# Kernel tuning notes

Hardware: AMD Instinct MI355X
Metric: run time of the kernel (lower is better)

The kernel has to match this reference:

```python
import jax, jax.numpy as jnp
import numpy as np

B, L, DIM, H = 2, 2048, 1024, 16
HD = DIM // H  # head dim = 64
MASK_SCALE = -10 * 6  # faithful to the original source: mask_expand *= -10 * 6


def setup_inputs() -> dict:
    key = jax.random.key(0)
    ks = jax.random.split(key, 8)
    s = 1.0 / np.sqrt(DIM)
    return {
        "x": jax.random.normal(ks[0], (B, L, DIM), jnp.float32),
        "attention_mask": jax.random.uniform(ks[1], (B, L, L), jnp.float32),
        "Wq": jax.random.normal(ks[2], (DIM, DIM), jnp.float32) * s,
        "bq": jnp.zeros((DIM,), jnp.float32),
        "Wk": jax.random.normal(ks[3], (DIM, DIM), jnp.float32) * s,
        "bk": jnp.zeros((DIM,), jnp.float32),
        "Wv": jax.random.normal(ks[4], (DIM, DIM), jnp.float32) * s,
        "bv": jnp.zeros((DIM,), jnp.float32),
    }


def _split_heads(t):
    # [B, L, DIM] -> [B, H, L, HD]
    return t.reshape(B, L, H, HD).transpose(0, 2, 1, 3)


def reference(x, attention_mask, Wq, bq, Wk, bk, Wv, bv):
    q = _split_heads(x @ Wq + bq)
    k = _split_heads(x @ Wk + bk)
    v = _split_heads(x @ Wv + bv)
    scale = float(HD) ** -0.5
    # full [B, H, L, L] score matrix, as in the original
    scores = jnp.einsum("bhqd,bhkd->bhqk", q, k) * scale
    scores = scores + attention_mask[:, None, :, :] * MASK_SCALE
    probs = jax.nn.softmax(scores, axis=-1)
    ctx = jnp.einsum("bhqk,bhkd->bhqd", probs, v)
    # merge heads back: [B, L, DIM]
    return ctx.transpose(0, 2, 1, 3).reshape(B, L, DIM)
```

## Files before the change

kernel.cpp:

```cpp
#include <hip/hip_runtime.h>

#define LL 2048
#define NHEADS 16
#define HDIM 64
#define QSCALE 0.18033688011112042f
#define MASKC1 -86.56170245333780f

typedef __attribute__((ext_vector_type(8))) __bf16 bf16x8;
typedef __attribute__((ext_vector_type(4))) float f32x4;

__device__ __forceinline__ unsigned short f2bf(float f) {
  unsigned int u = __builtin_bit_cast(unsigned int, f);
  u += 0x7fffu + ((u >> 16) & 1u);
  return (unsigned short)(u >> 16);
}

__device__ __forceinline__ bf16x8 ld_frag(const unsigned short* p) {
  return *reinterpret_cast<const bf16x8*>(p);
}

__device__ __forceinline__ void async_cp16(const unsigned short* g, unsigned short* l) {
  __builtin_amdgcn_global_load_lds(
      (const __attribute__((address_space(1))) unsigned int*)(unsigned long long)(g),
      (__attribute__((address_space(3))) unsigned int*)(unsigned int)(unsigned long long)(l),
      16, 0, 0);
}

__global__ __launch_bounds__(256) void prep_kernel(
    const float* __restrict__ x, const float* __restrict__ Wq, const float* __restrict__ Wk,
    const float* __restrict__ Wv, unsigned short* __restrict__ xb,
    unsigned short* __restrict__ WtAll) {
  __shared__ float t[64][65];
  int blk = blockIdx.x;
  if (blk < 4096) {
    int i = (blk * 256 + threadIdx.x) * 4;
    float4 v = *reinterpret_cast<const float4*>(x + i);
    ushort4 o;
    o.x = f2bf(v.x); o.y = f2bf(v.y); o.z = f2bf(v.z); o.w = f2bf(v.w);
    *reinterpret_cast<ushort4*>(xb + i) = o;
  } else {
    int idx = blk - 4096;
    int z = idx >> 8; idx &= 255;
    const float* W = (z == 0) ? Wq : (z == 1) ? Wk : Wv;
    unsigned short* dst = WtAll + (size_t)z * 1024 * 1024;
    int n0 = (idx & 15) * 64, k0 = (idx >> 4) * 64;
    int tx = threadIdx.x & 63, ty = threadIdx.x >> 6;
#pragma unroll
    for (int p = 0; p < 16; ++p) {
      int kr = p * 4 + ty;
      t[kr][tx] = W[(size_t)(k0 + kr) * 1024 + n0 + tx];
    }
    __syncthreads();
#pragma unroll
    for (int p = 0; p < 16; ++p) {
      int nr = p * 4 + ty;
      dst[(size_t)(n0 + nr) * 1024 + k0 + tx] = f2bf(t[tx][nr]);
    }
  }
}

__global__ __launch_bounds__(256) void em_prep_kernel(const float* __restrict__ mask,
                                                      unsigned short* __restrict__ em) {
  int row = blockIdx.y;
  int t = blockIdx.x * 256 + threadIdx.x;
  int kb = t >> 4, c = t & 15;
  const float* src = mask + (size_t)row * LL + kb * 64 + c;
  ushort4 o;
  o.x = f2bf(__builtin_amdgcn_exp2f(src[0]  * MASKC1));
  o.y = f2bf(__builtin_amdgcn_exp2f(src[16] * MASKC1));
  o.z = f2bf(__builtin_amdgcn_exp2f(src[32] * MASKC1));
  o.w = f2bf(__builtin_amdgcn_exp2f(src[48] * MASKC1));
  *reinterpret_cast<ushort4*>(em + (size_t)row * LL + kb * 64 + 4 * c) = o;
}

__global__ __launch_bounds__(256) void qkv_gemm_kernel(
    const unsigned short* __restrict__ xb, const unsigned short* __restrict__ WtAll,
    const float* __restrict__ bq, const float* __restrict__ bk, const float* __restrict__ bv,
    unsigned short* __restrict__ qkv) {
  const int z = blockIdx.z;
  const unsigned short* Wt = WtAll + (size_t)z * 1024 * 1024;
  const float* bias = (z == 0) ? bq : (z == 1) ? bk : bv;
  unsigned short* outb = qkv + (size_t)z * 4194304;

  __shared__ __align__(16) unsigned short smem[16384];
  unsigned short* As = smem;
  unsigned short* Bs = smem + 8192;

  const int tid = threadIdx.x;
  const int w = tid >> 6, lane = tid & 63, g = lane >> 4, cc = lane & 15;
  const int wm = w >> 1, wn = w & 1;
  const int m0 = blockIdx.y * 128, n0 = blockIdx.x * 128;
  const int srow = lane >> 3;
  const int gc = ((lane & 7) - srow) & 7;
  const unsigned short* ga = xb + (size_t)(m0 + w * 32 + srow) * 1024 + gc * 8;
  const unsigned short* gb = Wt + (size_t)(n0 + w * 32 + srow) * 1024 + gc * 8;
  unsigned short* la = As + w * 2048;
  unsigned short* lb = Bs + w * 2048;

  f32x4 acc[4][4];
#pragma unroll
  for (int i = 0; i < 4; ++i)
#pragma unroll
    for (int j = 0; j < 4; ++j) acc[i][j] = (f32x4)0.0f;

  for (int kk = 0; kk < 1024; kk += 64) {
    __syncthreads();
#pragma unroll
    for (int i = 0; i < 4; ++i) {
      async_cp16(ga + i * 8192 + kk, la + i * 512);
      async_cp16(gb + i * 8192 + kk, lb + i * 512);
    }
    __syncthreads();
    bf16x8 af[4][2], bfr[4][2];
#pragma unroll
    for (int mt = 0; mt < 4; ++mt)
#pragma unroll
      for (int ks = 0; ks < 2; ++ks)
        af[mt][ks] = ld_frag(&As[(wm * 64 + mt * 16 + cc) * 64 + ((4 * ks + g + cc) & 7) * 8]);
#pragma unroll
    for (int nt = 0; nt < 4; ++nt)
#pragma unroll
      for (int ks = 0; ks < 2; ++ks)
        bfr[nt][ks] = ld_frag(&Bs[(wn * 64 + nt * 16 + cc) * 64 + ((4 * ks + g + cc) & 7) * 8]);
#pragma unroll
    for (int mt = 0; mt < 4; ++mt)
#pragma unroll
      for (int nt = 0; nt < 4; ++nt)
#pragma unroll
        for (int ks = 0; ks < 2; ++ks)
          acc[mt][nt] = __builtin_amdgcn_mfma_f32_16x16x32_bf16(af[mt][ks], bfr[nt][ks],
                                                                acc[mt][nt], 0, 0, 0);
  }

  if (z != 2) {
    const float sc = (z == 0) ? QSCALE : 1.0f;
#pragma unroll
    for (int nt = 0; nt < 4; ++nt) {
      int n = n0 + wn * 64 + nt * 16 + cc;
      float bval = bias[n];
      int h = n >> 6, d = n & 63;
#pragma unroll
      for (int mt = 0; mt < 4; ++mt) {
#pragma unroll
        for (int r = 0; r < 4; ++r) {
          int m = m0 + wm * 64 + mt * 16 + g * 4 + r;
          int b = m >> 11, l = m & 2047;
          outb[(((size_t)(b * NHEADS + h) * LL) + l) * HDIM + d] =
              f2bf((acc[mt][nt][r] + bval) * sc);
        }
      }
    }
  } else {
    __syncthreads();
#pragma unroll
    for (int nt = 0; nt < 4; ++nt) {
      int nr = wn * 64 + nt * 16 + cc;
      float bval = bias[n0 + nr];
#pragma unroll
      for (int mt = 0; mt < 4; ++mt)
#pragma unroll
        for (int r = 0; r < 4; ++r)
          smem[nr * 128 + wm * 64 + 16 * g + 4 * r + mt] = f2bf(acc[mt][nt][r] + bval);
    }
    __syncthreads();
    int row = tid >> 1, half = tid & 1;
    int n = n0 + row, hh = n >> 6, dd = n & 63;
    int bb = m0 >> 11, l0 = (m0 & 2047) + half * 64;
    unsigned short* dst = outb + ((size_t)(bb * NHEADS + hh) * HDIM + dd) * LL + l0;
#pragma unroll
    for (int i = 0; i < 8; ++i)
      *reinterpret_cast<uint4*>(dst + i * 8) =
          *reinterpret_cast<const uint4*>(&smem[row * 128 + half * 64 + i * 8]);
  }
}

__global__ __launch_bounds__(256, 4) void flash_kernel(
    const unsigned short* __restrict__ Qb, const unsigned short* __restrict__ Kb,
    const unsigned short* __restrict__ Vt, const unsigned short* __restrict__ Em,
    float* __restrict__ out) {
  const int bh = blockIdx.y, b = bh >> 4, h = bh & 15;
  const int q0 = blockIdx.x * 64;
  const int tid = threadIdx.x, w = tid >> 6, lane = tid & 63, g = lane >> 4, cc = lane & 15;
  const size_t bhoff = (size_t)bh * LL * HDIM;

  __shared__ __align__(16) unsigned short Ps[64 * 64];
  __shared__ __align__(16) unsigned short Ks[2][64 * 64];
  __shared__ __align__(16) unsigned short Vs[2][64 * 64];

  bf16x8 aq[2];
#pragma unroll
  for (int ks = 0; ks < 2; ++ks)
    aq[ks] = *reinterpret_cast<const bf16x8*>(
        Qb + bhoff + (size_t)(q0 + w * 16 + cc) * HDIM + ks * 32 + g * 8);

  const int srow = lane >> 3;
  const int gcs = ((lane & 7) - srow) & 7;
  const unsigned short* kg0 = Kb + bhoff + (size_t)(w * 8 + srow) * HDIM + gcs * 8;
  const unsigned short* kg1 = Kb + bhoff + (size_t)(32 + w * 8 + srow) * HDIM + gcs * 8;
  const unsigned short* vg0 = Vt + bhoff + (size_t)(w * 8 + srow) * LL + gcs * 8;
  const unsigned short* vg1 = Vt + bhoff + (size_t)(32 + w * 8 + srow) * LL + gcs * 8;

  float li[4];
  f32x4 oacc[4];
#pragma unroll
  for (int r = 0; r < 4; ++r) li[r] = 0.0f;
#pragma unroll
  for (int nt = 0; nt < 4; ++nt) oacc[nt] = (f32x4)0.0f;

  const unsigned short* embase = Em + ((size_t)b * LL + q0 + w * 16) * LL + 4 * cc;

  async_cp16(kg0, Ks[0] + w * 512);
  async_cp16(kg1, Ks[0] + (w + 4) * 512);
  async_cp16(vg0, Vs[0] + w * 512);
  async_cp16(vg1, Vs[0] + (w + 4) * 512);

#pragma unroll 2
  for (int kt = 0; kt < 32; ++kt) {
    const int buf = kt & 1;
    __syncthreads();
    if (kt + 1 < 32) {
      const int nb = buf ^ 1;
      async_cp16(kg0 + (size_t)(kt + 1) * 64 * HDIM, Ks[nb] + w * 512);
      async_cp16(kg1 + (size_t)(kt + 1) * 64 * HDIM, Ks[nb] + (w + 4) * 512);
      async_cp16(vg0 + (kt + 1) * 64, Vs[nb] + w * 512);
      async_cp16(vg1 + (kt + 1) * 64, Vs[nb] + (w + 4) * 512);
    }
    uint2 emv[4];
#pragma unroll
    for (int r = 0; r < 4; ++r)
      emv[r] = *reinterpret_cast<const uint2*>(embase + (size_t)(g * 4 + r) * LL + kt * 64);

    bf16x8 bk_[4][2];
#pragma unroll
    for (int nt = 0; nt < 4; ++nt)
#pragma unroll
      for (int ks = 0; ks < 2; ++ks)
        bk_[nt][ks] = ld_frag(&Ks[buf][(nt * 16 + cc) * 64 + ((4 * ks + g + cc) & 7) * 8]);
    f32x4 sacc[4];
#pragma unroll
    for (int nt = 0; nt < 4; ++nt) sacc[nt] = (f32x4)0.0f;
#pragma unroll
    for (int nt = 0; nt < 4; ++nt)
#pragma unroll
      for (int ks = 0; ks < 2; ++ks)
        sacc[nt] = __builtin_amdgcn_mfma_f32_16x16x32_bf16(aq[ks], bk_[nt][ks], sacc[nt], 0, 0, 0);

#pragma unroll
    for (int r = 0; r < 4; ++r) {
      unsigned int ex = emv[r].x, ey = emv[r].y;
      float e0 = __builtin_bit_cast(float, ex << 16);
      float e1 = __builtin_bit_cast(float, ex & 0xffff0000u);
      float e2 = __builtin_bit_cast(float, ey << 16);
      float e3 = __builtin_bit_cast(float, ey & 0xffff0000u);
      float p0 = __builtin_amdgcn_exp2f(sacc[0][r]) * e0;
      float p1 = __builtin_amdgcn_exp2f(sacc[1][r]) * e1;
      float p2 = __builtin_amdgcn_exp2f(sacc[2][r]) * e2;
      float p3 = __builtin_amdgcn_exp2f(sacc[3][r]) * e3;
      unsigned int u01 = __builtin_amdgcn_perm(__builtin_bit_cast(unsigned int, p1),
                                               __builtin_bit_cast(unsigned int, p0),
                                               0x07060302u);
      unsigned int u23 = __builtin_amdgcn_perm(__builtin_bit_cast(unsigned int, p3),
                                               __builtin_bit_cast(unsigned int, p2),
                                               0x07060302u);
      li[r] += __builtin_bit_cast(float, u01 << 16) +
               __builtin_bit_cast(float, u01 & 0xffff0000u) +
               __builtin_bit_cast(float, u23 << 16) +
               __builtin_bit_cast(float, u23 & 0xffff0000u);
      uint2 pk; pk.x = u01; pk.y = u23;
      int prow = w * 16 + g * 4 + r;
      int poff = prow * 64 + ((((cc >> 1) + prow) & 7) << 3) + ((cc & 1) << 2);
      *reinterpret_cast<uint2*>(&Ps[poff]) = pk;
    }
    asm volatile("" ::: "memory");

    bf16x8 ap[2], bv[4][2];
    {
      int arow = w * 16 + cc;
#pragma unroll
      for (int ks = 0; ks < 2; ++ks)
        ap[ks] = ld_frag(&Ps[arow * 64 + (((ks * 4 + g + arow) & 7) << 3)]);
    }
#pragma unroll
    for (int nt = 0; nt < 4; ++nt)
#pragma unroll
      for (int ks = 0; ks < 2; ++ks)
        bv[nt][ks] = ld_frag(&Vs[buf][(nt * 16 + cc) * 64 + ((4 * ks + g + cc) & 7) * 8]);
#pragma unroll
    for (int nt = 0; nt < 4; ++nt)
#pragma unroll
      for (int ks = 0; ks < 2; ++ks)
        oacc[nt] = __builtin_amdgcn_mfma_f32_16x16x32_bf16(ap[ks], bv[nt][ks], oacc[nt], 0, 0, 0);
  }

#pragma unroll
  for (int r = 0; r < 4; ++r) {
    float s = li[r];
    s += __shfl_xor(s, 1);
    s += __shfl_xor(s, 2);
    s += __shfl_xor(s, 4);
    s += __shfl_xor(s, 8);
    float inv = 1.0f / s;
    int qrow = q0 + w * 16 + g * 4 + r;
#pragma unroll
    for (int nt = 0; nt < 4; ++nt)
      out[((size_t)b * LL + qrow) * 1024 + h * 64 + nt * 16 + cc] = oacc[nt][r] * inv;
  }
}

extern "C" void kernel_launch(void* const* d_in, const int* in_sizes, int n_in,
                              void* d_out, int out_size, void* d_ws, size_t ws_size,
                              hipStream_t stream) {
  const float* x    = (const float*)d_in[0];
  const float* mask = (const float*)d_in[1];
  const float* Wq   = (const float*)d_in[2];
  const float* bq   = (const float*)d_in[3];
  const float* Wk   = (const float*)d_in[4];
  const float* bk   = (const float*)d_in[5];
  const float* Wv   = (const float*)d_in[6];
  const float* bv   = (const float*)d_in[7];
  float* out = (float*)d_out;
  (void)in_sizes; (void)n_in; (void)out_size; (void)ws_size;

  char* ws = (char*)d_ws;
  unsigned short* qkv = (unsigned short*)(ws);
  unsigned short* xb  = (unsigned short*)(ws + (24u << 20));
  unsigned short* Wt  = (unsigned short*)(ws + (32u << 20));
  unsigned short* em  = (unsigned short*)(ws + (24u << 20));

  prep_kernel<<<dim3(4864), dim3(256), 0, stream>>>(x, Wq, Wk, Wv, xb, Wt);
  qkv_gemm_kernel<<<dim3(8, 32, 3), dim3(256), 0, stream>>>(xb, Wt, bq, bk, bv, qkv);
  em_prep_kernel<<<dim3(2, 4096), dim3(256), 0, stream>>>(mask, em);
  flash_kernel<<<dim3(32, 32), dim3(256), 0, stream>>>(qkv, qkv + 4194304, qkv + 8388608,
                                                       em, out);
}
```

Baseline: 214.9 us.

## Tile K/V/mask layouts so flash kernel loads fragments directly from global memory

Rewrites the QKV GEMM epilogue and the mask prep kernel to store K, V^T and exp(mask) in 64-wide key tiles, so each wave can load its MFMA fragments straight from global memory. The flash kernel drops the shared-memory K/V double buffer and its per-tile __syncthreads, keeping only a per-wave P scratch, and prefetches the next tile's K and mask into registers. The row sum is now computed with an extra MFMA against a ones vector instead of scalar adds and shuffles. The cost is more VGPR pressure (launch bound lowered to 3 waves) and reliance on L2/cache for K/V reuse across waves.

```diff
diff --git a/kernel.cpp b/kernel.cpp
--- a/kernel.cpp
+++ b/kernel.cpp
@@ -8,6 +8,7 @@
 
 typedef __attribute__((ext_vector_type(8))) __bf16 bf16x8;
 typedef __attribute__((ext_vector_type(4))) float f32x4;
+typedef __attribute__((ext_vector_type(4))) int i32x4;
 
 __device__ __forceinline__ unsigned short f2bf(float f) {
   unsigned int u = __builtin_bit_cast(unsigned int, f);
@@ -61,16 +62,18 @@
 
 __global__ __launch_bounds__(256) void em_prep_kernel(const float* __restrict__ mask,
                                                       unsigned short* __restrict__ em) {
-  int row = blockIdx.y;
-  int t = blockIdx.x * 256 + threadIdx.x;
-  int kb = t >> 4, c = t & 15;
-  const float* src = mask + (size_t)row * LL + kb * 64 + c;
+  unsigned int t = blockIdx.x * 256 + threadIdx.x;
+  int c = t & 15;
+  int q = (t >> 4) & 2047;
+  int kb = (t >> 15) & 31;
+  int b = t >> 20;
+  const float* src = mask + ((size_t)b * LL + q) * LL + kb * 64 + c;
   ushort4 o;
   o.x = f2bf(__builtin_amdgcn_exp2f(src[0]  * MASKC1));
   o.y = f2bf(__builtin_amdgcn_exp2f(src[16] * MASKC1));
   o.z = f2bf(__builtin_amdgcn_exp2f(src[32] * MASKC1));
   o.w = f2bf(__builtin_amdgcn_exp2f(src[48] * MASKC1));
-  *reinterpret_cast<ushort4*>(em + (size_t)row * LL + kb * 64 + 4 * c) = o;
+  *reinterpret_cast<ushort4*>(em + (((size_t)b * 32 + kb) * LL + q) * 64 + 4 * c) = o;
 }
 
 __global__ __launch_bounds__(256) void qkv_gemm_kernel(
@@ -165,8 +168,10 @@
     __syncthreads();
     int row = tid >> 1, half = tid & 1;
     int n = n0 + row, hh = n >> 6, dd = n & 63;
-    int bb = m0 >> 11, l0 = (m0 & 2047) + half * 64;
-    unsigned short* dst = outb + ((size_t)(bb * NHEADS + hh) * HDIM + dd) * LL + l0;
+    int bb = m0 >> 11;
+    int tI = ((m0 & 2047) >> 6) + half;
+    unsigned short* dst =
+        outb + (size_t)(bb * NHEADS + hh) * (LL * HDIM) + (size_t)tI * 4096 + dd * 64;
 #pragma unroll
     for (int i = 0; i < 8; ++i)
       *reinterpret_cast<uint4*>(dst + i * 8) =
@@ -174,76 +179,62 @@
   }
 }
 
-__global__ __launch_bounds__(256, 4) void flash_kernel(
+__global__ __launch_bounds__(256, 3) void flash_kernel(
     const unsigned short* __restrict__ Qb, const unsigned short* __restrict__ Kb,
     const unsigned short* __restrict__ Vt, const unsigned short* __restrict__ Em,
     float* __restrict__ out) {
   const int bh = blockIdx.y, b = bh >> 4, h = bh & 15;
   const int q0 = blockIdx.x * 64;
   const int tid = threadIdx.x, w = tid >> 6, lane = tid & 63, g = lane >> 4, cc = lane & 15;
-  const size_t bhoff = (size_t)bh * LL * HDIM;
-
-  __shared__ __align__(16) unsigned short Ps[64 * 64];
-  __shared__ __align__(16) unsigned short Ks[2][64 * 64];
-  __shared__ __align__(16) unsigned short Vs[2][64 * 64];
-
-  bf16x8 aq[2];
-#pragma unroll
-  for (int ks = 0; ks < 2; ++ks)
-    aq[ks] = *reinterpret_cast<const bf16x8*>(
-        Qb + bhoff + (size_t)(q0 + w * 16 + cc) * HDIM + ks * 32 + g * 8);
-
-  const int srow = lane >> 3;
-  const int gcs = ((lane & 7) - srow) & 7;
-  const unsigned short* kg0 = Kb + bhoff + (size_t)(w * 8 + srow) * HDIM + gcs * 8;
-  const unsigned short* kg1 = Kb + bhoff + (size_t)(32 + w * 8 + srow) * HDIM + gcs * 8;
-  const unsigned short* vg0 = Vt + bhoff + (size_t)(w * 8 + srow) * LL + gcs * 8;
-  const unsigned short* vg1 = Vt + bhoff + (size_t)(32 + w * 8 + srow) * LL + gcs * 8;
-
-  float li[4];
-  f32x4 oacc[4];
-#pragma unroll
-  for (int r = 0; r < 4; ++r) li[r] = 0.0f;
+  const size_t bhoff = (size_t)bh * (LL * HDIM);
+
+  __shared__ __align__(16) unsigned short Ps[4][16 * 64];
+  unsigned short* myP = Ps[w];
+
+  const unsigned short* qp = Qb + bhoff + (size_t)(q0 + w * 16 + cc) * HDIM + g * 8;
+  bf16x8 aq0 = ld_frag(qp);
+  bf16x8 aq1 = ld_frag(qp + 32);
+
+  const unsigned short* kpA = Kb + bhoff + cc * 64 + g * 8;
+  const unsigned short* kpB = kpA + 2048;
+  const unsigned short* vpA = Vt + bhoff + cc * 64 + g * 8;
+  const unsigned short* vpB = vpA + 2048;
+  const unsigned short* ep =
+      Em + ((size_t)b * 65536 + (q0 + w * 16 + g * 4)) * 64 + 4 * cc;
+
+  i32x4 onesi = {0x3F803F80, 0x3F803F80, 0x3F803F80, 0x3F803F80};
+  bf16x8 vones = __builtin_bit_cast(bf16x8, onesi);
+
+  f32x4 oacc[4], liacc;
 #pragma unroll
   for (int nt = 0; nt < 4; ++nt) oacc[nt] = (f32x4)0.0f;
-
-  const unsigned short* embase = Em + ((size_t)b * LL + q0 + w * 16) * LL + 4 * cc;
-
-  async_cp16(kg0, Ks[0] + w * 512);
-  async_cp16(kg1, Ks[0] + (w + 4) * 512);
-  async_cp16(vg0, Vs[0] + w * 512);
-  async_cp16(vg1, Vs[0] + (w + 4) * 512);
-
-#pragma unroll 2
+  liacc = (f32x4)0.0f;
+
+  bf16x8 bk[4][2];
+  bk[0][0] = ld_frag(kpA);        bk[0][1] = ld_frag(kpA + 32);
+  bk[1][0] = ld_frag(kpA + 1024); bk[1][1] = ld_frag(kpA + 1056);
+  bk[2][0] = ld_frag(kpB);        bk[2][1] = ld_frag(kpB + 32);
+  bk[3][0] = ld_frag(kpB + 1024); bk[3][1] = ld_frag(kpB + 1056);
+  uint2 emv[4];
+#pragma unroll
+  for (int r = 0; r < 4; ++r)
+    emv[r] = *reinterpret_cast<const uint2*>(ep + r * 64);
+
   for (int kt = 0; kt < 32; ++kt) {
-    const int buf = kt & 1;
-    __syncthreads();
-    if (kt + 1 < 32) {
-      const int nb = buf ^ 1;
-      async_cp16(kg0 + (size_t)(kt + 1) * 64 * HDIM, Ks[nb] + w * 512);
-      async_cp16(kg1 + (size_t)(kt + 1) * 64 * HDIM, Ks[nb] + (w + 4) * 512);
-      async_cp16(vg0 + (kt + 1) * 64, Vs[nb] + w * 512);
-      async_cp16(vg1 + (kt + 1) * 64, Vs[nb] + (w + 4) * 512);
-    }
-    uint2 emv[4];
-#pragma unroll
-    for (int r = 0; r < 4; ++r)
-      emv[r] = *reinterpret_cast<const uint2*>(embase + (size_t)(g * 4 + r) * LL + kt * 64);
-
-    bf16x8 bk_[4][2];
-#pragma unroll
-    for (int nt = 0; nt < 4; ++nt)
-#pragma unroll
-      for (int ks = 0; ks < 2; ++ks)
-        bk_[nt][ks] = ld_frag(&Ks[buf][(nt * 16 + cc) * 64 + ((4 * ks + g + cc) & 7) * 8]);
     f32x4 sacc[4];
 #pragma unroll
     for (int nt = 0; nt < 4; ++nt) sacc[nt] = (f32x4)0.0f;
 #pragma unroll
-    for (int nt = 0; nt < 4; ++nt)
-#pragma unroll
-      for (int ks = 0; ks < 2; ++ks)
-        sacc[nt] = __builtin_amdgcn_mfma_f32_16x16x32_bf16(aq[ks], bk_[nt][ks], sacc[nt], 0, 0, 0);
+    for (int nt = 0; nt < 4; ++nt) {
+      sacc[nt] = __builtin_amdgcn_mfma_f32_16x16x32_bf16(aq0, bk[nt][0], sacc[nt], 0, 0, 0);
+      sacc[nt] = __builtin_amdgcn_mfma_f32_16x16x32_bf16(aq1, bk[nt][1], sacc[nt], 0, 0, 0);
+    }
+
+    bf16x8 bv[4][2];
+    bv[0][0] = ld_frag(vpA);        bv[0][1] = ld_frag(vpA + 32);
+    bv[1][0] = ld_frag(vpA + 1024); bv[1][1] = ld_frag(vpA + 1056);
+    bv[2][0] = ld_frag(vpB);        bv[2][1] = ld_frag(vpB + 32);
+    bv[3][0] = ld_frag(vpB + 1024); bv[3][1] = ld_frag(vpB + 1056);
 
 #pragma unroll
     for (int r = 0; r < 4; ++r) {
@@ -262,44 +253,42 @@
       unsigned int u23 = __builtin_amdgcn_perm(__builtin_bit_cast(unsigned int, p3),
                                                __builtin_bit_cast(unsigned int, p2),
                                                0x07060302u);
-      li[r] += __builtin_bit_cast(float, u01 << 16) +
-               __builtin_bit_cast(float, u01 & 0xffff0000u) +
-               __builtin_bit_cast(float, u23 << 16) +
-               __builtin_bit_cast(float, u23 & 0xffff0000u);
       uint2 pk; pk.x = u01; pk.y = u23;
-      int prow = w * 16 + g * 4 + r;
-      int poff = prow * 64 + ((((cc >> 1) + prow) & 7) << 3) + ((cc & 1) << 2);
-      *reinterpret_cast<uint2*>(&Ps[poff]) = pk;
-    }
+      int prow = g * 4 + r;
+      *reinterpret_cast<uint2*>(
+          &myP[prow * 64 + ((((cc >> 1) + prow) & 7) << 3) + ((cc & 1) << 2)]) = pk;
+    }
+
+    const int adv = (kt < 31) ? 1 : 0;
+    kpA += adv * 4096; kpB += adv * 4096;
+    vpA += adv * 4096; vpB += adv * 4096;
+    ep += (size_t)adv * 131072;
+
+    bk[0][0] = ld_frag(kpA);        bk[0][1] = ld_frag(kpA + 32);
+    bk[1][0] = ld_frag(kpA + 1024); bk[1][1] = ld_frag(kpA + 1056);
+    bk[2][0] = ld_frag(kpB);        bk[2][1] = ld_frag(kpB + 32);
+    bk[3][0] = ld_frag(kpB + 1024); bk[3][1] = ld_frag(kpB + 1056);
+#pragma unroll
+    for (int r = 0; r < 4; ++r)
+      emv[r] = *reinterpret_cast<const uint2*>(ep + r * 64);
+
     asm volatile("" ::: "memory");
 
-    bf16x8 ap[2], bv[4][2];
-    {
-      int arow = w * 16 + cc;
-#pragma unroll
-      for (int ks = 0; ks < 2; ++ks)
-        ap[ks] = ld_frag(&Ps[arow * 64 + (((ks * 4 + g + arow) & 7) << 3)]);
-    }
-#pragma unroll
-    for (int nt = 0; nt < 4; ++nt)
-#pragma unroll
-      for (int ks = 0; ks < 2; ++ks)
-        bv[nt][ks] = ld_frag(&Vs[buf][(nt * 16 + cc) * 64 + ((4 * ks + g + cc) & 7) * 8]);
-#pragma unroll
-    for (int nt = 0; nt < 4; ++nt)
-#pragma unroll
-      for (int ks = 0; ks < 2; ++ks)
-        oacc[nt] = __builtin_amdgcn_mfma_f32_16x16x32_bf16(ap[ks], bv[nt][ks], oacc[nt], 0, 0, 0);
+    bf16x8 ap0 = ld_frag(&myP[cc * 64 + (((g + cc) & 7) << 3)]);
+    bf16x8 ap1 = ld_frag(&myP[cc * 64 + (((4 + g + cc) & 7) << 3)]);
+
+#pragma unroll
+    for (int nt = 0; nt < 4; ++nt) {
+      oacc[nt] = __builtin_amdgcn_mfma_f32_16x16x32_bf16(ap0, bv[nt][0], oacc[nt], 0, 0, 0);
+      oacc[nt] = __builtin_amdgcn_mfma_f32_16x16x32_bf16(ap1, bv[nt][1], oacc[nt], 0, 0, 0);
+    }
+    liacc = __builtin_amdgcn_mfma_f32_16x16x32_bf16(ap0, vones, liacc, 0, 0, 0);
+    liacc = __builtin_amdgcn_mfma_f32_16x16x32_bf16(ap1, vones, liacc, 0, 0, 0);
   }
 
 #pragma unroll
   for (int r = 0; r < 4; ++r) {
-    float s = li[r];
-    s += __shfl_xor(s, 1);
-    s += __shfl_xor(s, 2);
-    s += __shfl_xor(s, 4);
-    s += __shfl_xor(s, 8);
-    float inv = 1.0f / s;
+    float inv = 1.0f / liacc[r];
     int qrow = q0 + w * 16 + g * 4 + r;
 #pragma unroll
     for (int nt = 0; nt < 4; ++nt)
@@ -329,7 +318,7 @@
 
   prep_kernel<<<dim3(4864), dim3(256), 0, stream>>>(x, Wq, Wk, Wv, xb, Wt);
   qkv_gemm_kernel<<<dim3(8, 32, 3), dim3(256), 0, stream>>>(xb, Wt, bq, bk, bv, qkv);
-  em_prep_kernel<<<dim3(2, 4096), dim3(256), 0, stream>>>(mask, em);
+  em_prep_kernel<<<dim3(8192), dim3(256), 0, stream>>>(mask, em);
   flash_kernel<<<dim3(32, 32), dim3(256), 0, stream>>>(qkv, qkv + 4194304, qkv + 8388608,
                                                        em, out);
 }
```

Measured after the change: 396.6 us. 84.5% more time.
